# Kernel tuning notes

Hardware: AMD Instinct MI355X
Metric: run time of the kernel (lower is better)

Reference implementation:

```python
import jax, jax.numpy as jnp
import numpy as np

DIM = 512
HEADS = 8
DIM_HEAD = 64
INNER = HEADS * DIM_HEAD  # 512
EPS = 1e-5
SCALE = DIM_HEAD ** (-0.5)


def setup_inputs() -> dict:
    key = jax.random.key(0)
    ks = jax.random.split(key, 12)
    B, S = 8, 1024
    x = jax.random.normal(ks[0], (B, DIM, S, 1), dtype=jnp.float32)
    # BatchNorm2d params (eval mode: running stats)
    bn_gamma = jax.random.normal(ks[1], (DIM,), dtype=jnp.float32) * 0.1 + 1.0
    bn_beta = jax.random.normal(ks[2], (DIM,), dtype=jnp.float32) * 0.1
    bn_mean = jax.random.normal(ks[3], (DIM,), dtype=jnp.float32) * 0.1
    bn_var = jax.random.uniform(ks[4], (DIM,), dtype=jnp.float32, minval=0.5, maxval=1.5)
    # 1x1 Conv2d == linear: weight [out, in], bias [out]
    def lin(k, out_d, in_d):
        kw, kb = jax.random.split(k)
        lim = 1.0 / np.sqrt(in_d)
        w = jax.random.uniform(kw, (out_d, in_d), dtype=jnp.float32, minval=-lim, maxval=lim)
        b = jax.random.uniform(kb, (out_d,), dtype=jnp.float32, minval=-lim, maxval=lim)
        return w, b
    wq, bq = lin(ks[5], INNER, DIM)
    wk, bk = lin(ks[6], INNER, DIM)
    wv, bv = lin(ks[7], INNER, DIM)
    wo, bo = lin(ks[8], DIM, INNER)
    return {"x": x, "bn_gamma": bn_gamma, "bn_beta": bn_beta,
            "bn_mean": bn_mean, "bn_var": bn_var,
            "wq": wq, "bq": bq, "wk": wk, "bk": bk,
            "wv": wv, "bv": bv, "wo": wo, "bo": bo}


def reference(x, bn_gamma, bn_beta, bn_mean, bn_var,
              wq, bq, wk, bk, wv, bv, wo, bo):
    B, C, S, _ = x.shape
    # BatchNorm2d (eval) over channel dim
    inv = jax.lax.rsqrt(bn_var + EPS)
    xn = (x - bn_mean[None, :, None, None]) * (bn_gamma * inv)[None, :, None, None] \
         + bn_beta[None, :, None, None]
    t = jnp.transpose(xn[..., 0], (0, 2, 1))  # [B, S, C]
    q = (t @ wq.T + bq).reshape(B, S, HEADS, DIM_HEAD)
    k = (t @ wk.T + bk).reshape(B, S, HEADS, DIM_HEAD)
    v = (t @ wv.T + bv).reshape(B, S, HEADS, DIM_HEAD)
    scores = jnp.einsum('bshd,bthd->bhst', q, k) * SCALE  # [B,H,S,S]
    attn = jax.nn.softmax(scores, axis=-1)
    o = jnp.einsum('bhst,bthd->bshd', attn, v).reshape(B, S, INNER)
    y = o @ wo.T + bo  # [B, S, C]
    return jnp.transpose(y, (0, 2, 1))[..., None]  # [B, C, S, 1]
```

## Files before the change

### kernel.cpp

```cpp
#include <hip/hip_runtime.h>
#include <stdint.h>

typedef __bf16 bf16;
typedef bf16 bf16x8 __attribute__((ext_vector_type(8)));
typedef bf16 bf16x4 __attribute__((ext_vector_type(4)));
typedef float f32x4 __attribute__((ext_vector_type(4)));

#define NB 8
#define NS 1024
#define NC 512
#define NH 8
#define ND 64

#define QSCALE 0.18033688011f

__device__ __forceinline__ void gload16(const void* g, void* l) {
  __builtin_amdgcn_global_load_lds(
      (const __attribute__((address_space(1))) void*)g,
      (__attribute__((address_space(3))) void*)l, 16, 0, 0);
}

__global__ __launch_bounds__(256) void bn_tr_kernel(
    const float* __restrict__ x, const float* __restrict__ gam,
    const float* __restrict__ bet, const float* __restrict__ mu,
    const float* __restrict__ var, bf16* __restrict__ t) {
  __shared__ float tile[32][33];
  const int b = blockIdx.z, c0 = blockIdx.y * 32, s0 = blockIdx.x * 32;
  const int tx = threadIdx.x, sj = tx & 31, ci = tx >> 5;
#pragma unroll
  for (int kk = 0; kk < 4; ++kk) {
    const int c = c0 + ci + (kk << 3);
    const float sc = gam[c] * rsqrtf(var[c] + 1e-5f);
    const float sh = bet[c] - mu[c] * sc;
    tile[ci + (kk << 3)][sj] = x[(size_t)(b * NC + c) * NS + s0 + sj] * sc + sh;
  }
  __syncthreads();
#pragma unroll
  for (int kk = 0; kk < 4; ++kk) {
    const int s = s0 + ci + (kk << 3);
    t[(size_t)(b * NS + s) * NC + c0 + sj] = (bf16)tile[sj][ci + (kk << 3)];
  }
}

__global__ __launch_bounds__(256) void wconv_kernel(
    const float* __restrict__ wq, const float* __restrict__ wk,
    const float* __restrict__ wv, const float* __restrict__ wo,
    bf16* __restrict__ wqb, bf16* __restrict__ wkb, bf16* __restrict__ wvb,
    bf16* __restrict__ wob) {
  const int i = (blockIdx.x * 256 + threadIdx.x) * 4;
  float4 a = *(const float4*)(&wq[i]);
  float4 b = *(const float4*)(&wk[i]);
  float4 c = *(const float4*)(&wv[i]);
  float4 d = *(const float4*)(&wo[i]);
  bf16x4 av = {(bf16)a.x, (bf16)a.y, (bf16)a.z, (bf16)a.w};
  bf16x4 bv = {(bf16)b.x, (bf16)b.y, (bf16)b.z, (bf16)b.w};
  bf16x4 cv = {(bf16)c.x, (bf16)c.y, (bf16)c.z, (bf16)c.w};
  bf16x4 dv = {(bf16)d.x, (bf16)d.y, (bf16)d.z, (bf16)d.w};
  *(bf16x4*)(&wqb[i]) = av;
  *(bf16x4*)(&wkb[i]) = bv;
  *(bf16x4*)(&wvb[i]) = cv;
  *(bf16x4*)(&wob[i]) = dv;
}

__global__ __launch_bounds__(256) void gemm_qkv_kernel(
    const bf16* __restrict__ t, const bf16* __restrict__ wqb,
    const bf16* __restrict__ wkb, const bf16* __restrict__ wvb,
    const float* __restrict__ bq, const float* __restrict__ bk,
    const float* __restrict__ bv, bf16* __restrict__ qo, bf16* __restrict__ ko,
    bf16* __restrict__ vo) {
  __shared__ __align__(16) bf16 As[2][128 * 32];
  __shared__ __align__(16) bf16 Bs[2][128 * 32];
  const int tid = threadIdx.x;
  const int m0 = blockIdx.x * 128, n0 = blockIdx.y * 128;
  const int wsel = n0 >> 9;
  const bf16* W = (wsel == 0) ? wqb : (wsel == 1 ? wkb : wvb);
  const float* bias = (wsel == 0) ? bq : (wsel == 1 ? bk : bv);
  const int nb = n0 & 511;
  const int w = tid >> 6, lane = tid & 63, l15 = lane & 15, l4 = lane >> 4;
  const int wm = (w >> 1) << 6, wn = (w & 1) << 6;

  const int srl = lane >> 2, sp = lane & 3;
  const int r0 = w * 16 + srl, r1 = 64 + w * 16 + srl;
  const int c0off = (sp ^ ((r0 >> 1) & 3)) << 3;
  const int c1off = (sp ^ ((r1 >> 1) & 3)) << 3;
  const bf16* a0 = t + (size_t)(m0 + r0) * 512 + c0off;
  const bf16* a1 = t + (size_t)(m0 + r1) * 512 + c1off;
  const bf16* b0 = W + (size_t)(nb + r0) * 512 + c0off;
  const bf16* b1 = W + (size_t)(nb + r1) * 512 + c1off;

  f32x4 acc[4][4] = {};
  gload16(a0, &As[0][w * 512]);
  gload16(a1, &As[0][2048 + w * 512]);
  gload16(b0, &Bs[0][w * 512]);
  gload16(b1, &Bs[0][2048 + w * 512]);
  __syncthreads();
  int buf = 0;
  for (int k0 = 0; k0 < 512; k0 += 32, buf ^= 1) {
    if (k0 + 32 < 512) {
      gload16(a0 + k0 + 32, &As[buf ^ 1][w * 512]);
      gload16(a1 + k0 + 32, &As[buf ^ 1][2048 + w * 512]);
      gload16(b0 + k0 + 32, &Bs[buf ^ 1][w * 512]);
      gload16(b1 + k0 + 32, &Bs[buf ^ 1][2048 + w * 512]);
    }
    bf16x8 af[4], bfv[4];
#pragma unroll
    for (int mi = 0; mi < 4; ++mi) {
      const int row = wm + mi * 16 + l15;
      af[mi] = *(const bf16x8*)(&As[buf][row * 32 + ((l4 ^ ((row >> 1) & 3)) << 3)]);
    }
#pragma unroll
    for (int ni = 0; ni < 4; ++ni) {
      const int row = wn + ni * 16 + l15;
      bfv[ni] = *(const bf16x8*)(&Bs[buf][row * 32 + ((l4 ^ ((row >> 1) & 3)) << 3)]);
    }
    if (wsel == 2) {
#pragma unroll
      for (int mi = 0; mi < 4; ++mi)
#pragma unroll
        for (int ni = 0; ni < 4; ++ni)
          acc[mi][ni] = __builtin_amdgcn_mfma_f32_16x16x32_bf16(
              af[mi], bfv[ni], acc[mi][ni], 0, 0, 0);
    } else {
#pragma unroll
      for (int mi = 0; mi < 4; ++mi)
#pragma unroll
        for (int ni = 0; ni < 4; ++ni)
          acc[mi][ni] = __builtin_amdgcn_mfma_f32_16x16x32_bf16(
              bfv[ni], af[mi], acc[mi][ni], 0, 0, 0);
    }
    __syncthreads();
  }
  const int bidx = m0 >> 10;
  if (wsel == 2) {
    const int sbase = (m0 & 1023) + wm + (l4 << 2);
#pragma unroll
    for (int ni = 0; ni < 4; ++ni) {
      const int nn = nb + wn + ni * 16 + l15;
      const int hh = nn >> 6, dd = nn & 63;
      const float bsv = bias[nn];
      bf16* vbase = vo + (size_t)(bidx * NH + hh) * (ND * NS) + (size_t)dd * NS + sbase;
#pragma unroll
      for (int mi = 0; mi < 4; ++mi) {
        bf16x4 pk;
#pragma unroll
        for (int r = 0; r < 4; ++r) pk[r] = (bf16)(acc[mi][ni][r] + bsv);
        *(bf16x4*)(&vbase[mi * 16]) = pk;
      }
    }
  } else {
    const bool isq = (wsel == 0);
    bf16* outp = isq ? qo : ko;
    const int sbase = (m0 & 1023) + wm + l15;
#pragma unroll
    for (int ni = 0; ni < 4; ++ni) {
      const int nn0 = nb + wn + ni * 16 + (l4 << 2);
      const int hh = nn0 >> 6, dd0 = nn0 & 63;
      const float4 bs4 = *(const float4*)(&bias[nn0]);
      bf16* obase = outp + (size_t)(bidx * NH + hh) * (NS * ND) + dd0;
#pragma unroll
      for (int mi = 0; mi < 4; ++mi) {
        bf16x4 pk;
        const float* bp = (const float*)&bs4;
#pragma unroll
        for (int r = 0; r < 4; ++r) {
          float val = acc[mi][ni][r] + bp[r];
          if (isq) val *= QSCALE;
          pk[r] = (bf16)val;
        }
        *(bf16x4*)(&obase[(size_t)(sbase + mi * 16) * ND]) = pk;
      }
    }
  }
}

__global__ __launch_bounds__(512, 4) void attn_kernel(
    const bf16* __restrict__ qg, const bf16* __restrict__ kg,
    const bf16* __restrict__ vtg, bf16* __restrict__ og) {
  __shared__ __align__(16) bf16 Kb[2][128 * 64];
  __shared__ __align__(16) bf16 Vb[2][64 * 128];
  __shared__ __align__(16) bf16 Ps[8][16 * 64];
  const int bh = blockIdx.y, q0 = blockIdx.x * 128;
  const int tid = threadIdx.x, w = tid >> 6, lane = tid & 63;
  const int l15 = lane & 15, l4 = lane >> 4, l7 = l15 & 7;
  const bf16* Qp = qg + ((size_t)bh * NS + q0) * ND;
  const bf16* Kp = kg + (size_t)bh * NS * ND;
  const bf16* Vp = vtg + (size_t)bh * ND * NS;

  bf16x8 qf[2];
#pragma unroll
  for (int kk = 0; kk < 2; ++kk)
    qf[kk] = *(const bf16x8*)(&Qp[(size_t)(w * 16 + l15) * ND + ((kk << 2) + l4) * 8]);

  const int krow = w * 8 + (lane >> 3);
  const int kcol = ((lane & 7) ^ (krow & 7)) << 3;
  const bf16* ksrc = Kp + (size_t)krow * ND + kcol;
  const int vrow = w * 4 + (lane >> 4);
  const int vcol = ((lane & 15) ^ (vrow & 7)) << 3;
  const bf16* vsrc = Vp + (size_t)vrow * NS + vcol;

  f32x4 oacc[4] = {};
  float mrun = -1e30f, lrun = 0.f;

  gload16(ksrc, &Kb[0][w * 512]);
  gload16(ksrc + (size_t)64 * ND, &Kb[0][4096 + w * 512]);
  gload16(vsrc, &Vb[0][w * 512]);
  gload16(vsrc + (size_t)32 * NS, &Vb[0][4096 + w * 512]);
  __syncthreads();

  const int kb0 = l15 * 64 + ((l4 ^ l7) << 3);
  const int kb1 = l15 * 64 + (((4 + l4) ^ l7) << 3);
  int buf = 0;
  for (int kv0 = 0; kv0 < NS; kv0 += 128, buf ^= 1) {
    if (kv0 + 128 < NS) {
      gload16(ksrc + (size_t)(kv0 + 128) * ND, &Kb[buf ^ 1][w * 512]);
      gload16(ksrc + (size_t)(kv0 + 192) * ND, &Kb[buf ^ 1][4096 + w * 512]);
      gload16(vsrc + (kv0 + 128), &Vb[buf ^ 1][w * 512]);
      gload16(vsrc + (size_t)32 * NS + (kv0 + 128), &Vb[buf ^ 1][4096 + w * 512]);
    }
    const bf16* Ks = Kb[buf];
    const bf16* Vs = Vb[buf];
    f32x4 st[8];
    __builtin_amdgcn_s_setprio(1);
#pragma unroll
    for (int rt = 0; rt < 8; ++rt) {
      const bf16x8 a0 = *(const bf16x8*)(&Ks[rt * 1024 + kb0]);
      const bf16x8 a1 = *(const bf16x8*)(&Ks[rt * 1024 + kb1]);
      f32x4 z = {0.f, 0.f, 0.f, 0.f};
      z = __builtin_amdgcn_mfma_f32_16x16x32_bf16(a0, qf[0], z, 0, 0, 0);
      st[rt] = __builtin_amdgcn_mfma_f32_16x16x32_bf16(a1, qf[1], z, 0, 0, 0);
    }
    __builtin_amdgcn_s_setprio(0);
    float pm = -1e30f;
#pragma unroll
    for (int rt = 0; rt < 8; ++rt)
#pragma unroll
      for (int r = 0; r < 4; ++r) pm = fmaxf(pm, st[rt][r]);
    pm = fmaxf(pm, __shfl_xor(pm, 16));
    pm = fmaxf(pm, __shfl_xor(pm, 32));
    if (!__all(pm - mrun <= 8.f)) {
      const float mnew = fmaxf(mrun, pm);
      const float alpha = __builtin_amdgcn_exp2f(mrun - mnew);
#pragma unroll
      for (int di = 0; di < 4; ++di)
#pragma unroll
        for (int r = 0; r < 4; ++r) oacc[di][r] *= alpha;
      lrun *= alpha;
      mrun = mnew;
    }
    float rs = 0.f;
#pragma unroll
    for (int h = 0; h < 2; ++h) {
#pragma unroll
      for (int rt4 = 0; rt4 < 4; ++rt4) {
        const int rt = h * 4 + rt4;
        bf16x4 pk;
#pragma unroll
        for (int r = 0; r < 4; ++r) {
          const float p = __builtin_amdgcn_exp2f(st[rt][r] - mrun);
          rs += p;
          pk[r] = (bf16)p;
        }
        const int slot = (rt4 << 1) + (l4 >> 1);
        *(bf16x4*)(&Ps[w][l15 * 64 + ((slot ^ l7) << 3) + ((l4 & 1) << 2)]) = pk;
      }
      bf16x8 pa0 = *(const bf16x8*)(&Ps[w][l15 * 64 + ((l4 ^ l7) << 3)]);
      bf16x8 pa1 = *(const bf16x8*)(&Ps[w][l15 * 64 + (((4 + l4) ^ l7) << 3)]);
      __builtin_amdgcn_s_setprio(1);
#pragma unroll
      for (int di = 0; di < 4; ++di) {
        const int vb = (di * 16 + l15) * 128;
        const bf16x8 v0 =
            *(const bf16x8*)(&Vs[vb + ((((h << 3) + l4) ^ l7) << 3)]);
        const bf16x8 v1 =
            *(const bf16x8*)(&Vs[vb + ((((h << 3) + 4 + l4) ^ l7) << 3)]);
        oacc[di] = __builtin_amdgcn_mfma_f32_16x16x32_bf16(v0, pa0, oacc[di], 0, 0, 0);
        oacc[di] = __builtin_amdgcn_mfma_f32_16x16x32_bf16(v1, pa1, oacc[di], 0, 0, 0);
      }
      __builtin_amdgcn_s_setprio(0);
    }
    lrun += rs;
    __syncthreads();
  }
  lrun += __shfl_xor(lrun, 16);
  lrun += __shfl_xor(lrun, 32);
  const float linv = 1.f / lrun;
  const int b = bh >> 3, h = bh & 7;
  bf16* Op = og + (size_t)(b * NS + q0 + w * 16 + l15) * NC + h * ND + (l4 << 2);
#pragma unroll
  for (int di = 0; di < 4; ++di) {
    bf16x4 pk;
#pragma unroll
    for (int r = 0; r < 4; ++r) pk[r] = (bf16)(oacc[di][r] * linv);
    *(bf16x4*)(&Op[di * 16]) = pk;
  }
}

__global__ __launch_bounds__(256) void gemm_out_kernel(
    const bf16* __restrict__ wob, const bf16* __restrict__ o,
    const float* __restrict__ bo, float* __restrict__ out) {
  __shared__ __align__(16) bf16 As[2][128 * 32];
  __shared__ __align__(16) bf16 Bs[2][128 * 32];
  const int tid = threadIdx.x;
  const int m0 = blockIdx.x * 128, n0 = blockIdx.y * 128;
  const int w = tid >> 6, lane = tid & 63, l15 = lane & 15, l4 = lane >> 4;
  const int wm = (w >> 1) << 6, wn = (w & 1) << 6;

  const int srl = lane >> 2, sp = lane & 3;
  const int r0 = w * 16 + srl, r1 = 64 + w * 16 + srl;
  const int c0off = (sp ^ ((r0 >> 1) & 3)) << 3;
  const int c1off = (sp ^ ((r1 >> 1) & 3)) << 3;
  const bf16* a0 = wob + (size_t)(m0 + r0) * 512 + c0off;
  const bf16* a1 = wob + (size_t)(m0 + r1) * 512 + c1off;
  const bf16* b0 = o + (size_t)(n0 + r0) * 512 + c0off;
  const bf16* b1 = o + (size_t)(n0 + r1) * 512 + c1off;

  f32x4 acc[4][4] = {};
  gload16(a0, &As[0][w * 512]);
  gload16(a1, &As[0][2048 + w * 512]);
  gload16(b0, &Bs[0][w * 512]);
  gload16(b1, &Bs[0][2048 + w * 512]);
  __syncthreads();
  int buf = 0;
  for (int k0 = 0; k0 < 512; k0 += 32, buf ^= 1) {
    if (k0 + 32 < 512) {
      gload16(a0 + k0 + 32, &As[buf ^ 1][w * 512]);
      gload16(a1 + k0 + 32, &As[buf ^ 1][2048 + w * 512]);
      gload16(b0 + k0 + 32, &Bs[buf ^ 1][w * 512]);
      gload16(b1 + k0 + 32, &Bs[buf ^ 1][2048 + w * 512]);
    }
    bf16x8 af[4], bfv[4];
#pragma unroll
    for (int mi = 0; mi < 4; ++mi) {
      const int row = wm + mi * 16 + l15;
      af[mi] = *(const bf16x8*)(&As[buf][row * 32 + ((l4 ^ ((row >> 1) & 3)) << 3)]);
    }
#pragma unroll
    for (int ni = 0; ni < 4; ++ni) {
      const int row = wn + ni * 16 + l15;
      bfv[ni] = *(const bf16x8*)(&Bs[buf][row * 32 + ((l4 ^ ((row >> 1) & 3)) << 3)]);
    }
#pragma unroll
    for (int mi = 0; mi < 4; ++mi)
#pragma unroll
      for (int ni = 0; ni < 4; ++ni)
        acc[mi][ni] = __builtin_amdgcn_mfma_f32_16x16x32_bf16(
            bfv[ni], af[mi], acc[mi][ni], 0, 0, 0);
    __syncthreads();
  }
  const int b = n0 >> 10;
  const int sb = (n0 & 1023) + wn;
#pragma unroll
  for (int mi = 0; mi < 4; ++mi) {
    const int cout = m0 + wm + mi * 16 + l15;
    const float bsv = bo[cout];
    float* obase = out + (size_t)(b * NC + cout) * NS;
#pragma unroll
    for (int ni = 0; ni < 4; ++ni) {
      const int s0i = sb + ni * 16 + (l4 << 2);
      float4 pk = {acc[mi][ni][0] + bsv, acc[mi][ni][1] + bsv,
                   acc[mi][ni][2] + bsv, acc[mi][ni][3] + bsv};
      *(float4*)(&obase[s0i]) = pk;
    }
  }
}

extern "C" void kernel_launch(void* const* d_in, const int* in_sizes, int n_in,
                              void* d_out, int out_size, void* d_ws,
                              size_t ws_size, hipStream_t stream) {
  const float* x = (const float*)d_in[0];
  const float* gam = (const float*)d_in[1];
  const float* bet = (const float*)d_in[2];
  const float* mu = (const float*)d_in[3];
  const float* var = (const float*)d_in[4];
  const float* wq = (const float*)d_in[5];
  const float* bq = (const float*)d_in[6];
  const float* wk = (const float*)d_in[7];
  const float* bk = (const float*)d_in[8];
  const float* wv = (const float*)d_in[9];
  const float* bv = (const float*)d_in[10];
  const float* wo = (const float*)d_in[11];
  const float* bo = (const float*)d_in[12];
  float* out = (float*)d_out;

  char* p = (char*)d_ws;
  const size_t big = (size_t)8192 * 512 * sizeof(bf16);
  bf16* t = (bf16*)p;   p += big;
  bf16* q = (bf16*)p;   p += big;
  bf16* k = (bf16*)p;   p += big;
  bf16* vt = (bf16*)p;  p += big;
  const size_t wsz = (size_t)512 * 512 * sizeof(bf16);
  bf16* wqb = (bf16*)p; p += wsz;
  bf16* wkb = (bf16*)p; p += wsz;
  bf16* wvb = (bf16*)p; p += wsz;
  bf16* wob = (bf16*)p; p += wsz;
  bf16* o = t;

  bn_tr_kernel<<<dim3(32, 16, 8), 256, 0, stream>>>(x, gam, bet, mu, var, t);
  wconv_kernel<<<dim3(256), 256, 0, stream>>>(wq, wk, wv, wo, wqb, wkb, wvb, wob);
  gemm_qkv_kernel<<<dim3(64, 12), 256, 0, stream>>>(t, wqb, wkb, wvb, bq, bk, bv,
                                                    q, k, vt);
  attn_kernel<<<dim3(8, 64), 512, 0, stream>>>(q, k, vt, o);
  gemm_out_kernel<<<dim3(4, 64), 256, 0, stream>>>(wob, o, bo, out);
}
```

Before: 93.09 us.

## Remap block IDs for XCD-aware L2 locality and shrink attention KV tile

The QKV, attention and output GEMM kernels now launch on a 1D grid. Each block ID is remapped so that blocks landing on the same XCD (lid & 7) share operands, for example the same batch-head's K/V or the same weight tile, which should improve L2 hit rates on the chiplet design. The attention kernel also drops its KV tile from 128 to 64 rows per iteration. This halves the LDS footprint and simplifies the P·V loop, at the cost of twice as many iterations and __syncthreads barriers.

```diff
diff --git a/kernel.cpp b/kernel.cpp
--- a/kernel.cpp
+++ b/kernel.cpp
@@ -70,8 +70,11 @@
     bf16* __restrict__ vo) {
   __shared__ __align__(16) bf16 As[2][128 * 32];
   __shared__ __align__(16) bf16 Bs[2][128 * 32];
+  const int lid = blockIdx.x;
+  const int xcd = lid & 7, rr = lid >> 3;
+  const int ny = rr % 12, mx = (rr / 12) * 8 + xcd;
+  const int m0 = mx << 7, n0 = ny << 7;
   const int tid = threadIdx.x;
-  const int m0 = blockIdx.x * 128, n0 = blockIdx.y * 128;
   const int wsel = n0 >> 9;
   const bf16* W = (wsel == 0) ? wqb : (wsel == 1 ? wkb : wvb);
   const float* bias = (wsel == 0) ? bq : (wsel == 1 ? bk : bv);
@@ -176,10 +179,13 @@
 __global__ __launch_bounds__(512, 4) void attn_kernel(
     const bf16* __restrict__ qg, const bf16* __restrict__ kg,
     const bf16* __restrict__ vtg, bf16* __restrict__ og) {
-  __shared__ __align__(16) bf16 Kb[2][128 * 64];
-  __shared__ __align__(16) bf16 Vb[2][64 * 128];
+  __shared__ __align__(16) bf16 Kb[2][64 * 64];
+  __shared__ __align__(16) bf16 Vb[2][64 * 64];
   __shared__ __align__(16) bf16 Ps[8][16 * 64];
-  const int bh = blockIdx.y, q0 = blockIdx.x * 128;
+  const int lid = blockIdx.x;
+  const int xcd = lid & 7, rr = lid >> 3;
+  const int bh = ((rr & 7) << 3) + xcd;
+  const int q0 = (rr >> 3) << 7;
   const int tid = threadIdx.x, w = tid >> 6, lane = tid & 63;
   const int l15 = lane & 15, l4 = lane >> 4, l7 = l15 & 7;
   const bf16* Qp = qg + ((size_t)bh * NS + q0) * ND;
@@ -191,40 +197,33 @@
   for (int kk = 0; kk < 2; ++kk)
     qf[kk] = *(const bf16x8*)(&Qp[(size_t)(w * 16 + l15) * ND + ((kk << 2) + l4) * 8]);
 
-  const int krow = w * 8 + (lane >> 3);
-  const int kcol = ((lane & 7) ^ (krow & 7)) << 3;
-  const bf16* ksrc = Kp + (size_t)krow * ND + kcol;
-  const int vrow = w * 4 + (lane >> 4);
-  const int vcol = ((lane & 15) ^ (vrow & 7)) << 3;
-  const bf16* vsrc = Vp + (size_t)vrow * NS + vcol;
+  const int srow = w * 8 + (lane >> 3);
+  const int scol = ((lane & 7) ^ (srow & 7)) << 3;
+  const bf16* ksrc = Kp + (size_t)srow * ND + scol;
+  const bf16* vsrc = Vp + (size_t)srow * NS + scol;
 
   f32x4 oacc[4] = {};
   float mrun = -1e30f, lrun = 0.f;
 
   gload16(ksrc, &Kb[0][w * 512]);
-  gload16(ksrc + (size_t)64 * ND, &Kb[0][4096 + w * 512]);
   gload16(vsrc, &Vb[0][w * 512]);
-  gload16(vsrc + (size_t)32 * NS, &Vb[0][4096 + w * 512]);
   __syncthreads();
 
-  const int kb0 = l15 * 64 + ((l4 ^ l7) << 3);
-  const int kb1 = l15 * 64 + (((4 + l4) ^ l7) << 3);
   int buf = 0;
-  for (int kv0 = 0; kv0 < NS; kv0 += 128, buf ^= 1) {
-    if (kv0 + 128 < NS) {
-      gload16(ksrc + (size_t)(kv0 + 128) * ND, &Kb[buf ^ 1][w * 512]);
-      gload16(ksrc + (size_t)(kv0 + 192) * ND, &Kb[buf ^ 1][4096 + w * 512]);
-      gload16(vsrc + (kv0 + 128), &Vb[buf ^ 1][w * 512]);
-      gload16(vsrc + (size_t)32 * NS + (kv0 + 128), &Vb[buf ^ 1][4096 + w * 512]);
+  for (int kv0 = 0; kv0 < NS; kv0 += 64, buf ^= 1) {
+    if (kv0 + 64 < NS) {
+      gload16(ksrc + (size_t)(kv0 + 64) * ND, &Kb[buf ^ 1][w * 512]);
+      gload16(vsrc + (kv0 + 64), &Vb[buf ^ 1][w * 512]);
     }
     const bf16* Ks = Kb[buf];
     const bf16* Vs = Vb[buf];
-    f32x4 st[8];
+    f32x4 st[4];
     __builtin_amdgcn_s_setprio(1);
 #pragma unroll
-    for (int rt = 0; rt < 8; ++rt) {
-      const bf16x8 a0 = *(const bf16x8*)(&Ks[rt * 1024 + kb0]);
-      const bf16x8 a1 = *(const bf16x8*)(&Ks[rt * 1024 + kb1]);
+    for (int rt = 0; rt < 4; ++rt) {
+      const int rb = (rt * 16 + l15) * 64;
+      const bf16x8 a0 = *(const bf16x8*)(&Ks[rb + ((l4 ^ l7) << 3)]);
+      const bf16x8 a1 = *(const bf16x8*)(&Ks[rb + (((4 + l4) ^ l7) << 3)]);
       f32x4 z = {0.f, 0.f, 0.f, 0.f};
       z = __builtin_amdgcn_mfma_f32_16x16x32_bf16(a0, qf[0], z, 0, 0, 0);
       st[rt] = __builtin_amdgcn_mfma_f32_16x16x32_bf16(a1, qf[1], z, 0, 0, 0);
@@ -232,7 +231,7 @@
     __builtin_amdgcn_s_setprio(0);
     float pm = -1e30f;
 #pragma unroll
-    for (int rt = 0; rt < 8; ++rt)
+    for (int rt = 0; rt < 4; ++rt)
 #pragma unroll
       for (int r = 0; r < 4; ++r) pm = fmaxf(pm, st[rt][r]);
     pm = fmaxf(pm, __shfl_xor(pm, 16));
@@ -249,36 +248,30 @@
     }
     float rs = 0.f;
 #pragma unroll
-    for (int h = 0; h < 2; ++h) {
-#pragma unroll
-      for (int rt4 = 0; rt4 < 4; ++rt4) {
-        const int rt = h * 4 + rt4;
-        bf16x4 pk;
-#pragma unroll
-        for (int r = 0; r < 4; ++r) {
-          const float p = __builtin_amdgcn_exp2f(st[rt][r] - mrun);
-          rs += p;
-          pk[r] = (bf16)p;
-        }
-        const int slot = (rt4 << 1) + (l4 >> 1);
-        *(bf16x4*)(&Ps[w][l15 * 64 + ((slot ^ l7) << 3) + ((l4 & 1) << 2)]) = pk;
+    for (int rt = 0; rt < 4; ++rt) {
+      bf16x4 pk;
+#pragma unroll
+      for (int r = 0; r < 4; ++r) {
+        const float p = __builtin_amdgcn_exp2f(st[rt][r] - mrun);
+        rs += p;
+        pk[r] = (bf16)p;
       }
-      bf16x8 pa0 = *(const bf16x8*)(&Ps[w][l15 * 64 + ((l4 ^ l7) << 3)]);
-      bf16x8 pa1 = *(const bf16x8*)(&Ps[w][l15 * 64 + (((4 + l4) ^ l7) << 3)]);
-      __builtin_amdgcn_s_setprio(1);
-#pragma unroll
-      for (int di = 0; di < 4; ++di) {
-        const int vb = (di * 16 + l15) * 128;
-        const bf16x8 v0 =
-            *(const bf16x8*)(&Vs[vb + ((((h << 3) + l4) ^ l7) << 3)]);
-        const bf16x8 v1 =
-            *(const bf16x8*)(&Vs[vb + ((((h << 3) + 4 + l4) ^ l7) << 3)]);
-        oacc[di] = __builtin_amdgcn_mfma_f32_16x16x32_bf16(v0, pa0, oacc[di], 0, 0, 0);
-        oacc[di] = __builtin_amdgcn_mfma_f32_16x16x32_bf16(v1, pa1, oacc[di], 0, 0, 0);
-      }
-      __builtin_amdgcn_s_setprio(0);
+      const int slot = (rt << 1) + (l4 >> 1);
+      *(bf16x4*)(&Ps[w][l15 * 64 + ((slot ^ l7) << 3) + ((l4 & 1) << 2)]) = pk;
     }
     lrun += rs;
+    const bf16x8 pa0 = *(const bf16x8*)(&Ps[w][l15 * 64 + ((l4 ^ l7) << 3)]);
+    const bf16x8 pa1 = *(const bf16x8*)(&Ps[w][l15 * 64 + (((4 + l4) ^ l7) << 3)]);
+    __builtin_amdgcn_s_setprio(1);
+#pragma unroll
+    for (int di = 0; di < 4; ++di) {
+      const int vb = (di * 16 + l15) * 64;
+      const bf16x8 v0 = *(const bf16x8*)(&Vs[vb + ((l4 ^ l7) << 3)]);
+      const bf16x8 v1 = *(const bf16x8*)(&Vs[vb + (((4 + l4) ^ l7) << 3)]);
+      oacc[di] = __builtin_amdgcn_mfma_f32_16x16x32_bf16(v0, pa0, oacc[di], 0, 0, 0);
+      oacc[di] = __builtin_amdgcn_mfma_f32_16x16x32_bf16(v1, pa1, oacc[di], 0, 0, 0);
+    }
+    __builtin_amdgcn_s_setprio(0);
     __syncthreads();
   }
   lrun += __shfl_xor(lrun, 16);
@@ -300,8 +293,11 @@
     const float* __restrict__ bo, float* __restrict__ out) {
   __shared__ __align__(16) bf16 As[2][128 * 32];
   __shared__ __align__(16) bf16 Bs[2][128 * 32];
+  const int lid = blockIdx.x;
+  const int xcd = lid & 7, rr = lid >> 3;
+  const int mx = rr & 3, ny = ((rr >> 2) << 3) + xcd;
+  const int m0 = mx << 7, n0 = ny << 7;
   const int tid = threadIdx.x;
-  const int m0 = blockIdx.x * 128, n0 = blockIdx.y * 128;
   const int w = tid >> 6, lane = tid & 63, l15 = lane & 15, l4 = lane >> 4;
   const int wm = (w >> 1) << 6, wn = (w & 1) << 6;
 
@@ -397,8 +393,8 @@
 
   bn_tr_kernel<<<dim3(32, 16, 8), 256, 0, stream>>>(x, gam, bet, mu, var, t);
   wconv_kernel<<<dim3(256), 256, 0, stream>>>(wq, wk, wv, wo, wqb, wkb, wvb, wob);
-  gemm_qkv_kernel<<<dim3(64, 12), 256, 0, stream>>>(t, wqb, wkb, wvb, bq, bk, bv,
-                                                    q, k, vt);
-  attn_kernel<<<dim3(8, 64), 512, 0, stream>>>(q, k, vt, o);
-  gemm_out_kernel<<<dim3(4, 64), 256, 0, stream>>>(wob, o, bo, out);
-}
+  gemm_qkv_kernel<<<dim3(768), 256, 0, stream>>>(t, wqb, wkb, wvb, bq, bk, bv,
+                                                 q, k, vt);
+  attn_kernel<<<dim3(512), 512, 0, stream>>>(q, k, vt, o);
+  gemm_out_kernel<<<dim3(256), 256, 0, stream>>>(wob, o, bo, out);
+}
```

Result: faster. 87.91 us (-5.6%).
